# Optimization experiments

Hardware: AMD Instinct MI355X
Metric: run time of the kernel (lower is better)

## Reference

```python
import jax, jax.numpy as jnp
from jax import lax
import numpy as np

VOCAB = 2048
EMB = 256
LAT = 128
MAX_SENLEN = 8
SIZE_LAT = 3.0
BATCH = 32


def lm_softmax(tokens, E, Wi, Wh, b):
    """Embedding(mask_zero) -> LSTM(units=VOCAB) -> softmax. tokens: [B, L] int."""
    B, L = tokens.shape
    emb = E[tokens]                      # [B, L, EMB]
    mask = (tokens != 0)                 # PAD==0 is masked (Keras mask_zero)
    H = Wh.shape[0]

    def step(carry, xm):
        h, c = carry
        x, m = xm                        # x: [B, EMB], m: [B]
        gates = x @ Wi + h @ Wh + b      # [B, 4H], Keras gate order i,f,g,o
        i, f, g, o = jnp.split(gates, 4, axis=1)
        i = jax.nn.sigmoid(i)
        f = jax.nn.sigmoid(f)
        g = jnp.tanh(g)
        o = jax.nn.sigmoid(o)
        c_new = f * c + i * g
        h_new = o * jnp.tanh(c_new)
        m = m[:, None]
        h = jnp.where(m, h_new, h)       # masked steps carry state through
        c = jnp.where(m, c_new, c)
        return (h, c), None

    h0 = jnp.zeros((B, H), emb.dtype)
    (h, _), _ = lax.scan(step, (h0, h0), (jnp.swapaxes(emb, 0, 1), mask.T))
    return jax.nn.softmax(h, axis=-1)    # [B, VOCAB]


def setup_inputs() -> dict:
    key = jax.random.key(0)
    k1, k2, k3, k4 = jax.random.split(key, 4)
    input_tokens = jax.random.randint(k1, (BATCH, MAX_SENLEN), 0, VOCAB, dtype=jnp.int32)
    E = jax.random.normal(k2, (VOCAB, EMB), jnp.float32) * 0.02
    Wi = jax.random.normal(k3, (EMB, 4 * VOCAB), jnp.float32) * 0.02
    Wh = jax.random.normal(k4, (VOCAB, 4 * VOCAB), jnp.float32) * 0.02
    b = jnp.zeros((4 * VOCAB,), jnp.float32).at[VOCAB:2 * VOCAB].set(1.0)  # unit_forget_bias
    return {"input_tokens": input_tokens, "E": E, "Wi": Wi, "Wh": Wh, "b": b}


def reference(input_tokens, E, Wi, Wh, b):
    """Unrolled DAriEL_Encoder_Cell_2 RNN: returns z sequence [B, T, LAT]."""
    B, T = input_tokens.shape
    tokens = jnp.zeros((B, T + 1), jnp.int32)        # tokens state, col 0 = PAD
    # RNN zero initial state: bounds both zero at t=0 (cond keeps them since timeStep==0)
    low = jnp.zeros((B, LAT), jnp.float32)
    upp = jnp.zeros((B, LAT), jnp.float32)
    outs = []
    for t in range(T):
        # replace_column(tokens, input_token, timeStep+1)
        tokens = tokens.at[:, t + 1].set(input_tokens[:, t])
        if t > 0:  # tf.cond(mean(timeStep) > 0, initial bounds, state bounds)
            low = jnp.zeros((B, LAT), jnp.float32)
            upp = jnp.full((B, LAT), SIZE_LAT, jnp.float32)
        sm = lm_softmax(tokens[:, : t + 1], E, Wi, Wh, b)   # LM on prefix s_0toj
        s_j = tokens[:, t + 1]                               # current token
        c_inc = jnp.cumsum(sm, axis=1)
        c_exc = c_inc - sm
        cu = jnp.take_along_axis(c_inc, s_j[:, None], axis=1)  # [B,1]
        cl = jnp.take_along_axis(c_exc, s_j[:, None], axis=1)  # [B,1]
        rng = upp - low
        new_low = low + rng * cl
        upp = low + rng * cu
        low = new_low
        z = (low + upp) * 0.5            # mean over stacked bounds
        outs.append(z)
    return jnp.stack(outs, axis=1)       # [B, T, LAT]
```

## Files before the change

kernel.cpp:

```cpp
#include <hip/hip_runtime.h>

#define BATCH 32
#define TT 8
#define VOCAB 2048
#define EMB 256
#define NG 8192
#define LAT 128
#define KTOT 2304
#define NKT 72
#define NJT 128

#define WSCALE 4096.0f
#define ASCALE 16.0f
#define DQ (1.0f/65536.0f)

typedef float f32x4 __attribute__((ext_vector_type(4)));

#define EAC_OFF 0
#define FLG_OFF 256
#define ZP_OFF  4352
#define SP_OFF  33024
#define AFX_OFF 61696
#define AFH_OFF 76032
#define BP_OFF  108800

#define AT_LD(p)    __hip_atomic_load((p),  __ATOMIC_RELAXED, __HIP_MEMORY_SCOPE_AGENT)
#define AT_ST(p,v)  __hip_atomic_store((p), (v), __ATOMIC_RELAXED, __HIP_MEMORY_SCOPE_AGENT)

__device__ __forceinline__ float sigmoidf_(float x){ return 1.f/(1.f+__expf(-x)); }
__device__ __forceinline__ float tanhf_(float x){
  x = fminf(fmaxf(x, -10.f), 10.f);
  float e = __expf(2.f*x);
  return (e-1.f)/(e+1.f);
}
__device__ __forceinline__ unsigned char f2e4m3(float f){
  unsigned int u = __float_as_uint(f);
  unsigned char sign = (unsigned char)((u >> 24) & 0x80);
  float a = fabsf(f);
  if (a >= 464.f) return sign | 0x7E;
  if (a < 0.015625f){
    float q = rintf(a * 512.f);
    if (q >= 8.f) return sign | 0x08;
    return sign | (unsigned char)q;
  }
  int e;
  frexpf(a, &e);
  int E = e - 1;
  float q = rintf(ldexpf(a, 3 - E));
  int qi = (int)q;
  if (qi == 16){ qi = 8; E += 1; }
  if (E > 8) return sign | 0x7E;
  if (E == 8 && qi > 14) qi = 14;
  return sign | (unsigned char)(((E + 7) << 3) | (qi - 8));
}

__global__ __launch_bounds__(256) void k_pack(
    const int* __restrict__ tok, const float* __restrict__ E,
    const float* __restrict__ Wi, const float* __restrict__ Wh,
    unsigned long long* __restrict__ Bp,
    unsigned long long* __restrict__ AfX, unsigned long long* __restrict__ AfH1,
    int* __restrict__ flg, float* __restrict__ out){
  const int tid = threadIdx.x;
  const int nb = blockIdx.x;
  const int kt = blockIdx.y;
  __shared__ unsigned char lds[32][64];
  {
    const int kl = tid >> 3;
    const int n0 = (tid & 7) * 8;
    const int k  = kt*32 + kl;
    const float* W = (k < EMB) ? (Wi + (size_t)k*NG) : (Wh + (size_t)(k-EMB)*NG);
    const float4 f0 = *(const float4*)(W + nb*64 + n0);
    const float4 f1 = *(const float4*)(W + nb*64 + n0 + 4);
    unsigned long long pk = 0ull;
    pk |= (unsigned long long)f2e4m3(f0.x*WSCALE);
    pk |= (unsigned long long)f2e4m3(f0.y*WSCALE) << 8;
    pk |= (unsigned long long)f2e4m3(f0.z*WSCALE) << 16;
    pk |= (unsigned long long)f2e4m3(f0.w*WSCALE) << 24;
    pk |= (unsigned long long)f2e4m3(f1.x*WSCALE) << 32;
    pk |= (unsigned long long)f2e4m3(f1.y*WSCALE) << 40;
    pk |= (unsigned long long)f2e4m3(f1.z*WSCALE) << 48;
    pk |= (unsigned long long)f2e4m3(f1.w*WSCALE) << 56;
    *(unsigned long long*)&lds[kl][n0] = pk;
  }
  __syncthreads();
  {
    const int ntl = tid >> 6, lane = tid & 63;
    const int kgrp = lane >> 4, n16 = lane & 15;
    unsigned long long pk = 0ull;
    #pragma unroll
    for (int p=0;p<8;p++)
      pk |= ((unsigned long long)lds[kgrp*8 + p][ntl*16 + n16]) << (8*p);
    Bp[((size_t)(nb*4 + ntl)*NKT + kt)*64 + lane] = pk;
  }
  const int i = (kt*128 + nb)*256 + tid;
  if (i < 7*32*32){
    const int s   = i >> 10;
    const int rem = i & 1023;
    const int b   = rem >> 5;
    const int kgi = rem & 31;
    const int tk  = tok[b*TT + s];
    const float4 e0 = *(const float4*)(E + (size_t)tk*EMB + kgi*8);
    const float4 e1 = *(const float4*)(E + (size_t)tk*EMB + kgi*8 + 4);
    unsigned long long pk = 0ull;
    pk |= (unsigned long long)f2e4m3(e0.x*ASCALE);
    pk |= (unsigned long long)f2e4m3(e0.y*ASCALE) << 8;
    pk |= (unsigned long long)f2e4m3(e0.z*ASCALE) << 16;
    pk |= (unsigned long long)f2e4m3(e0.w*ASCALE) << 24;
    pk |= (unsigned long long)f2e4m3(e1.x*ASCALE) << 32;
    pk |= (unsigned long long)f2e4m3(e1.y*ASCALE) << 40;
    pk |= (unsigned long long)f2e4m3(e1.z*ASCALE) << 48;
    pk |= (unsigned long long)f2e4m3(e1.w*ASCALE) << 56;
    AfX[((size_t)((s*2 + (b>>4))*8 + (kgi>>2)))*64 + (kgi&3)*16 + (b&15)] = pk;
  }
  if (i < 8192) AfH1[i] = 0ull;
  if (i < BATCH*LAT)
    out[(size_t)((i>>7)*TT + 0)*LAT + (i&(LAT-1))] = 0.f;
  if (i < 4096) flg[i] = 0;
}

__global__ __launch_bounds__(256, 1) void k_fused(
    const int* __restrict__ tok, const float* __restrict__ bias,
    float* __restrict__ out, float* __restrict__ Zp, float* __restrict__ Sp,
    float* __restrict__ Eac, const unsigned long long* __restrict__ AfX,
    unsigned long long* __restrict__ AfH, const unsigned long long* __restrict__ Bp,
    int* __restrict__ flg){
  const int tid = threadIdx.x;
  const int bid = blockIdx.x;
  const int jt = bid & 127, mh = bid >> 7;
  const int g = tid >> 6, lane = tid & 63;
  const int quad = lane >> 4, col = lane & 15;

  __shared__ float gsh[4][16][16];
  __shared__ unsigned char hsh[256];
  __shared__ float zsh[2];

  const long* __restrict__ BpV = (const long*)Bp;
  const size_t bbase = (size_t)(g*NJT + jt)*NKT*64 + lane;
  long Breg[NKT];
  #pragma unroll
  for (int i=0;i<NKT;i++) Breg[i] = BpV[bbase + (size_t)i*64];
  #pragma unroll
  for (int i=0;i<NKT;i++) asm volatile("" : "+v"(Breg[i]));

  const int b16 = tid >> 4, jj = tid & 15;
  const int b = mh*16 + b16;
  const int j = jt*16 + jj;
  const float bi  = bias[j];
  const float bff = bias[j + VOCAB];
  const float bgg = bias[j + 2*VOCAB];
  const float boo = bias[j + 3*VOCAB];
  const int hoff = ((jj>>3)&1)*128 + b16*8 + (jj&7);
  const size_t bofs = (size_t)(mh*64 + (jt>>1))*512 + (size_t)(jt&1)*256;
  float hreg = 0.f, creg = 0.f;

  for (int t=1; t<TT; t++){
    if (t >= 2){
      const int want = t-1;
      while (AT_LD(&flg[tid*16]) < want) __builtin_amdgcn_s_sleep(1);
      asm volatile("" ::: "memory");
      __syncthreads();
      if (bid < BATCH){
        const int s = t-2;
        if (tid < 64){
          float zl = AT_LD(&Zp[((size_t)s*32+bid)*128 + tid])
                   + AT_LD(&Zp[((size_t)s*32+bid)*128 + tid + 64]);
          float sl = AT_LD(&Sp[((size_t)s*32+bid)*128 + tid])
                   + AT_LD(&Sp[((size_t)s*32+bid)*128 + tid + 64]);
          #pragma unroll
          for (int m=1; m<64; m<<=1){ zl += __shfl_xor(zl, m); sl += __shfl_xor(sl, m); }
          if (tid == 0){ zsh[0] = zl; zsh[1] = sl; }
        }
        __syncthreads();
        if (tid < LAT){
          const float Ej = AT_LD(&Eac[s*32 + bid]);
          out[((size_t)bid*TT + (t-1))*LAT + tid] = (3.f*zsh[1] + 1.5f*Ej)/zsh[0];
        }
      }
    }

    const long* __restrict__ aX = (const long*)AfX + (size_t)((t-1)*2 + mh)*512 + lane;
    unsigned long long* aH = AfH + (size_t)(t&1)*8192 + (size_t)mh*4096 + lane;
    long ah[64];
    #pragma unroll
    for (int i=0;i<64;i++) ah[i] = (long)AT_LD(&aH[(size_t)i*64]);
    f32x4 acc = {0,0,0,0};
    #pragma unroll
    for (int kt=0; kt<8; kt++)
      acc = __builtin_amdgcn_mfma_f32_16x16x32_fp8_fp8(aX[(size_t)kt*64], Breg[kt], acc, 0,0,0);
    #pragma unroll
    for (int kt=8; kt<NKT; kt++)
      acc = __builtin_amdgcn_mfma_f32_16x16x32_fp8_fp8(ah[kt-8], Breg[kt], acc, 0,0,0);
    #pragma unroll
    for (int r=0;r<4;r++) gsh[g][quad*4 + r][col] = acc[r];
    __syncthreads();

    const float ip = gsh[0][b16][jj]*DQ + bi;
    const float fp = gsh[1][b16][jj]*DQ + bff;
    const float gg = gsh[2][b16][jj]*DQ + bgg;
    const float op = gsh[3][b16][jj]*DQ + boo;
    const float cn = sigmoidf_(fp)*creg + sigmoidf_(ip)*tanhf_(gg);
    const float hn = sigmoidf_(op)*tanhf_(cn);
    if (tok[b*TT + (t-1)] != 0){ hreg = hn; creg = cn; }
    hsh[hoff] = f2e4m3(ASCALE*hreg);
    const int sj = tok[b*TT + t];
    const float e = __expf(hreg);
    if (j == sj) AT_ST(&Eac[(t-1)*32 + b], e);
    float z = e, s = (j < sj) ? e : 0.f;
    #pragma unroll
    for (int m=1; m<16; m<<=1){ z += __shfl_xor(z, m); s += __shfl_xor(s, m); }
    if (jj == 0){
      AT_ST(&Zp[((size_t)(t-1)*32 + b)*128 + jt], z);
      AT_ST(&Sp[((size_t)(t-1)*32 + b)*128 + jt], s);
    }
    __syncthreads();
    if (tid < 32){
      unsigned long long* dst =
        (unsigned long long*)((unsigned char*)AfH + (size_t)((t&1)^1)*65536 + bofs);
      AT_ST(&dst[tid], ((const unsigned long long*)hsh)[tid]);
    }
    asm volatile("s_waitcnt vmcnt(0)" ::: "memory");
    __syncthreads();
    if (tid == 0) AT_ST(&flg[bid*16], t);
  }

  if (bid < BATCH){
    while (AT_LD(&flg[tid*16]) < TT-1) __builtin_amdgcn_s_sleep(1);
    asm volatile("" ::: "memory");
    __syncthreads();
    const int s = TT-2;
    if (tid < 64){
      float zl = AT_LD(&Zp[((size_t)s*32+bid)*128 + tid])
               + AT_LD(&Zp[((size_t)s*32+bid)*128 + tid + 64]);
      float sl = AT_LD(&Sp[((size_t)s*32+bid)*128 + tid])
               + AT_LD(&Sp[((size_t)s*32+bid)*128 + tid + 64]);
      #pragma unroll
      for (int m=1; m<64; m<<=1){ zl += __shfl_xor(zl, m); sl += __shfl_xor(sl, m); }
      if (tid == 0){ zsh[0] = zl; zsh[1] = sl; }
    }
    __syncthreads();
    if (tid < LAT){
      const float Ej = AT_LD(&Eac[s*32 + bid]);
      out[((size_t)bid*TT + (TT-1))*LAT + tid] = (3.f*zsh[1] + 1.5f*Ej)/zsh[0];
    }
  }
}

extern "C" void kernel_launch(void* const* d_in, const int* in_sizes, int n_in,
                              void* d_out, int out_size, void* d_ws, size_t ws_size,
                              hipStream_t stream){
  const int*   tok  = (const int*)d_in[0];
  const float* E    = (const float*)d_in[1];
  const float* Wi   = (const float*)d_in[2];
  const float* Wh   = (const float*)d_in[3];
  const float* bias = (const float*)d_in[4];
  float* out = (float*)d_out;
  float* ws  = (float*)d_ws;
  float* Eac = ws + EAC_OFF;
  int*   flg = (int*)(ws + FLG_OFF);
  float* Zp  = ws + ZP_OFF;
  float* Sp  = ws + SP_OFF;
  unsigned long long* AfX = (unsigned long long*)(ws + AFX_OFF);
  unsigned long long* AfH = (unsigned long long*)(ws + AFH_OFF);
  unsigned long long* Bp  = (unsigned long long*)(ws + BP_OFF);

  k_pack<<<dim3(128, NKT), 256, 0, stream>>>(tok, E, Wi, Wh, Bp, AfX, AfH + 8192,
                                             flg, out);
  k_fused<<<256, 256, 0, stream>>>(tok, bias, out, Zp, Sp, Eac, AfX, AfH, Bp, flg);
}
```

Before: 162.8 us.

## Overlap input MFMAs with barrier wait, stage h via LDS, bitwise fp8 convert

The input-projection MFMAs now run before the grid-wide flag wait, so they overlap with waiting on other blocks. The spin loop is confined to one wavefront, which checks four flags per lane. Each wave then loads a quarter of the recurrent h activations from global memory and shares them through LDS, replacing 64 per-lane atomic loads in every wave. The per-step output normalisation is moved after the flag publish, taking it off the critical path, and the fp8 e4m3 conversion is replaced by bit-manipulation rounding. The cost is 32KB of extra LDS, two more block barriers per step, and possible small rounding differences in the new conversion.

```diff
diff --git a/kernel.cpp b/kernel.cpp
--- a/kernel.cpp
+++ b/kernel.cpp
@@ -34,24 +34,16 @@
   return (e-1.f)/(e+1.f);
 }
 __device__ __forceinline__ unsigned char f2e4m3(float f){
-  unsigned int u = __float_as_uint(f);
-  unsigned char sign = (unsigned char)((u >> 24) & 0x80);
-  float a = fabsf(f);
-  if (a >= 464.f) return sign | 0x7E;
-  if (a < 0.015625f){
-    float q = rintf(a * 512.f);
-    if (q >= 8.f) return sign | 0x08;
-    return sign | (unsigned char)q;
-  }
-  int e;
-  frexpf(a, &e);
-  int E = e - 1;
-  float q = rintf(ldexpf(a, 3 - E));
-  int qi = (int)q;
-  if (qi == 16){ qi = 8; E += 1; }
-  if (E > 8) return sign | 0x7E;
-  if (E == 8 && qi > 14) qi = 14;
-  return sign | (unsigned char)(((E + 7) << 3) | (qi - 8));
+  const unsigned int u = __float_as_uint(f);
+  const unsigned int sign = (u >> 24) & 0x80u;
+  const unsigned int au = u & 0x7FFFFFFFu;
+  const unsigned int r = au + 0x0007FFFFu + ((au >> 20) & 1u);
+  unsigned int code = (((r >> 23) - 120u) << 3) | ((r >> 20) & 7u);
+  code = (code > 0x7Eu) ? 0x7Eu : code;
+  const float a = __uint_as_float(au);
+  const unsigned int sub = (unsigned int)rintf(a * 512.0f);
+  code = (au < 0x3C800000u) ? sub : code;
+  return (unsigned char)(sign | code);
 }
 
 __global__ __launch_bounds__(256) void k_pack(
@@ -131,6 +123,7 @@
   const int quad = lane >> 4, col = lane & 15;
 
   __shared__ float gsh[4][16][16];
+  __shared__ long hlds[64][64];
   __shared__ unsigned char hsh[256];
   __shared__ float zsh[2];
 
@@ -154,42 +147,42 @@
   float hreg = 0.f, creg = 0.f;
 
   for (int t=1; t<TT; t++){
+    const long* __restrict__ aX = (const long*)AfX + (size_t)((t-1)*2 + mh)*512 + lane;
+    f32x4 acc = {0,0,0,0};
+    #pragma unroll
+    for (int kt=0; kt<8; kt++)
+      acc = __builtin_amdgcn_mfma_f32_16x16x32_fp8_fp8(aX[(size_t)kt*64], Breg[kt], acc, 0,0,0);
+
     if (t >= 2){
       const int want = t-1;
-      while (AT_LD(&flg[tid*16]) < want) __builtin_amdgcn_s_sleep(1);
-      asm volatile("" ::: "memory");
-      __syncthreads();
-      if (bid < BATCH){
-        const int s = t-2;
-        if (tid < 64){
-          float zl = AT_LD(&Zp[((size_t)s*32+bid)*128 + tid])
-                   + AT_LD(&Zp[((size_t)s*32+bid)*128 + tid + 64]);
-          float sl = AT_LD(&Sp[((size_t)s*32+bid)*128 + tid])
-                   + AT_LD(&Sp[((size_t)s*32+bid)*128 + tid + 64]);
+      if (tid < 64){
+        for (;;){
+          int done = 1;
           #pragma unroll
-          for (int m=1; m<64; m<<=1){ zl += __shfl_xor(zl, m); sl += __shfl_xor(sl, m); }
-          if (tid == 0){ zsh[0] = zl; zsh[1] = sl; }
-        }
-        __syncthreads();
-        if (tid < LAT){
-          const float Ej = AT_LD(&Eac[s*32 + bid]);
-          out[((size_t)bid*TT + (t-1))*LAT + tid] = (3.f*zsh[1] + 1.5f*Ej)/zsh[0];
+          for (int q2=0;q2<4;q2++)
+            done &= (AT_LD(&flg[(tid*4+q2)*16]) >= want) ? 1 : 0;
+          if (done) break;
+          __builtin_amdgcn_s_sleep(2);
         }
       }
-    }
-
-    const long* __restrict__ aX = (const long*)AfX + (size_t)((t-1)*2 + mh)*512 + lane;
-    unsigned long long* aH = AfH + (size_t)(t&1)*8192 + (size_t)mh*4096 + lane;
-    long ah[64];
-    #pragma unroll
-    for (int i=0;i<64;i++) ah[i] = (long)AT_LD(&aH[(size_t)i*64]);
-    f32x4 acc = {0,0,0,0};
-    #pragma unroll
-    for (int kt=0; kt<8; kt++)
-      acc = __builtin_amdgcn_mfma_f32_16x16x32_fp8_fp8(aX[(size_t)kt*64], Breg[kt], acc, 0,0,0);
+      asm volatile("" ::: "memory");
+    }
+    __syncthreads();
+
+    {
+      unsigned long long* aH = AfH + (size_t)(t&1)*8192 + (size_t)mh*4096;
+      long hl[16];
+      #pragma unroll
+      for (int i=0;i<16;i++)
+        hl[i] = (long)AT_LD(&aH[(size_t)(g*16+i)*64 + lane]);
+      #pragma unroll
+      for (int i=0;i<16;i++) hlds[g*16+i][lane] = hl[i];
+    }
+    __syncthreads();
+
     #pragma unroll
     for (int kt=8; kt<NKT; kt++)
-      acc = __builtin_amdgcn_mfma_f32_16x16x32_fp8_fp8(ah[kt-8], Breg[kt], acc, 0,0,0);
+      acc = __builtin_amdgcn_mfma_f32_16x16x32_fp8_fp8(hlds[kt-8][lane], Breg[kt], acc, 0,0,0);
     #pragma unroll
     for (int r=0;r<4;r++) gsh[g][quad*4 + r][col] = acc[r];
     __syncthreads();
@@ -213,6 +206,7 @@
       AT_ST(&Sp[((size_t)(t-1)*32 + b)*128 + jt], s);
     }
     __syncthreads();
+
     if (tid < 32){
       unsigned long long* dst =
         (unsigned long long*)((unsigned char*)AfH + (size_t)((t&1)^1)*65536 + bofs);
@@ -221,6 +215,24 @@
     asm volatile("s_waitcnt vmcnt(0)" ::: "memory");
     __syncthreads();
     if (tid == 0) AT_ST(&flg[bid*16], t);
+
+    if (t >= 2 && bid < BATCH){
+      const int s = t-2;
+      if (tid < 64){
+        float zl = AT_LD(&Zp[((size_t)s*32+bid)*128 + tid])
+                 + AT_LD(&Zp[((size_t)s*32+bid)*128 + tid + 64]);
+        float sl = AT_LD(&Sp[((size_t)s*32+bid)*128 + tid])
+                 + AT_LD(&Sp[((size_t)s*32+bid)*128 + tid + 64]);
+        #pragma unroll
+        for (int m=1; m<64; m<<=1){ zl += __shfl_xor(zl, m); sl += __shfl_xor(sl, m); }
+        if (tid == 0){ zsh[0] = zl; zsh[1] = sl; }
+      }
+      __syncthreads();
+      if (tid < LAT){
+        const float Ej = AT_LD(&Eac[s*32 + bid]);
+        out[((size_t)bid*TT + (t-1))*LAT + tid] = (3.f*zsh[1] + 1.5f*Ej)/zsh[0];
+      }
+    }
   }
 
   if (bid < BATCH){
```

After: 141.0 us. -13.4%, faster.
